# Kernel optimization log

Hardware: AMD Instinct MI355X
Metric: run time of the kernel (lower is better)

## Reference

```python
import jax, jax.numpy as jnp
import numpy as np
from jax import lax

EPS = 1e-5
K = 7
G = 4


def _dwconv_bn(x, w, g, b, m, v):
    # depthwise 3x3, pad 1, then BN (eval mode with running stats)
    C = x.shape[1]
    y = lax.conv_general_dilated(x, w, (1, 1), [(1, 1), (1, 1)],
                                 feature_group_count=C,
                                 dimension_numbers=('NCHW', 'OIHW', 'NCHW'))
    scale = (g / jnp.sqrt(v + EPS))[None, :, None, None]
    return (y - m[None, :, None, None]) * scale + b[None, :, None, None]


def _proj(t, pw1, pb1, pw2, pb2):
    # 1x1 conv -> GELU(exact) -> 1x1 conv, on small spatial maps
    h = jnp.einsum('bchw,oc->bohw', t, pw1) + pb1[None, :, None, None]
    h = jax.nn.gelu(h, approximate=False)
    return jnp.einsum('bchw,oc->bohw', h, pw2) + pb2[None, :, None, None]


def setup_inputs() -> dict:
    key = jax.random.key(0)
    ks = jax.random.split(key, 17)
    B, C, H, W = 16, 256, 56, 56
    r = C // 4
    inp = {
        'x1': jax.random.normal(ks[0], (B, C, H, W), jnp.float32),
        'dw1_w': jax.random.normal(ks[1], (C, 1, 3, 3), jnp.float32) * 0.1,
        'dw1_g': jax.random.uniform(ks[2], (C,), jnp.float32, 0.5, 1.5),
        'dw1_b': jax.random.normal(ks[3], (C,), jnp.float32) * 0.1,
        'dw1_m': jax.random.normal(ks[4], (C,), jnp.float32) * 0.1,
        'dw1_v': jax.random.uniform(ks[5], (C,), jnp.float32, 0.5, 1.5),
        'dw2_w': jax.random.normal(ks[6], (C, 1, 3, 3), jnp.float32) * 0.1,
        'dw2_g': jax.random.uniform(ks[7], (C,), jnp.float32, 0.5, 1.5),
        'dw2_b': jax.random.normal(ks[8], (C,), jnp.float32) * 0.1,
        'dw2_m': jax.random.normal(ks[9], (C,), jnp.float32) * 0.1,
        'dw2_v': jax.random.uniform(ks[10], (C,), jnp.float32, 0.5, 1.5),
        'weight1': jax.random.normal(ks[11], (G, C, K, K), jnp.float32) * 0.02,
        'bias1': jax.random.normal(ks[12], (G, C), jnp.float32) * 0.02,
        'pw1': jax.random.normal(ks[13], (r, C), jnp.float32) * 0.05,
        'pb1': jax.random.normal(ks[14], (r,), jnp.float32) * 0.05,
        'pw2': jax.random.normal(ks[15], (C * G, r), jnp.float32) * 0.05,
        'pb2': jax.random.normal(ks[16], (C * G,), jnp.float32) * 0.05,
    }
    return inp


def reference(x1, dw1_w, dw1_g, dw1_b, dw1_m, dw1_v,
              dw2_w, dw2_g, dw2_b, dw2_m, dw2_v,
              weight1, bias1, pw1, pb1, pw2, pb2):
    B, C, H, W = x1.shape
    # gated fuse: relu6(dw1(x)) * dw2(x)
    a = jnp.clip(_dwconv_bn(x1, dw1_w, dw1_g, dw1_b, dw1_m, dw1_v), 0.0, 6.0)
    x_fuse = a * _dwconv_bn(x1, dw2_w, dw2_g, dw2_b, dw2_m, dw2_v)

    # adaptive avg pool to (K,K): H,W multiples of K -> uniform block means
    pooled = x_fuse.reshape(B, C, K, H // K, K, W // K).mean(axis=(3, 5))

    # dynamic kernel: proj -> softmax over groups -> weighted sum of weight1
    scale1 = _proj(pooled, pw1, pb1, pw2, pb2).reshape(B, G, C, K, K)
    scale1 = jax.nn.softmax(scale1, axis=1)
    w_dyn = jnp.sum(scale1 * weight1[None], axis=1)  # [B, C, K, K]

    # dynamic bias
    mean_x = x_fuse.mean(axis=(-2, -1), keepdims=True)  # [B, C, 1, 1]
    sb = _proj(mean_x, pw1, pb1, pw2, pb2).reshape(B, G, C)
    sb = jax.nn.softmax(sb, axis=1)
    b_dyn = jnp.sum(sb * bias1[None], axis=1)  # [B, C]

    # per-sample depthwise conv with dynamic weights
    pad = K // 2

    def per_sample(xi, wi):  # xi [C,H,W], wi [C,K,K]
        y = lax.conv_general_dilated(xi[None], wi[:, None], (1, 1),
                                     [(pad, pad), (pad, pad)],
                                     feature_group_count=C,
                                     dimension_numbers=('NCHW', 'OIHW', 'NCHW'))
        return y[0]

    out = jax.vmap(per_sample)(x_fuse, w_dyn)  # [B, C, H, W]
    return out + b_dyn[:, :, None, None]
```

## Files before the change

kernel.cpp:

```cpp
#include <hip/hip_runtime.h>
#include <math.h>

#define BATCH 16
#define CH 256
#define HW 56
#define NPIX (HW*HW)

__device__ __forceinline__ void fuse_tile(
    const float* __restrict__ plane, int ty, int tx,
    const float w1[9], const float w2[9],
    float sc1, float be1, float sc2, float be2,
    float res[4][4])
{
    const int oy = 4 * ty;
    float y1a[4][4], y2a[4][4];
    #pragma unroll
    for (int a = 0; a < 4; a++)
        #pragma unroll
        for (int e = 0; e < 4; e++) { y1a[a][e] = 0.f; y2a[a][e] = 0.f; }

    #pragma unroll
    for (int iy = 0; iy < 6; iy++) {
        const int r    = oy - 1 + iy;
        const bool rok = (r >= 0) && (r < 56);
        const int rc   = rok ? r : 0;
        float rb[12];
        #pragma unroll
        for (int k = 0; k < 3; k++) {
            const int cx  = tx - 1 + k;
            const bool cv = (cx >= 0) && (cx < 14);
            const int cc2 = cv ? cx : 0;
            const bool ok = rok && cv;
            float4 v = *(const float4*)(plane + rc*56 + 4*cc2);
            rb[4*k+0] = ok ? v.x : 0.f;
            rb[4*k+1] = ok ? v.y : 0.f;
            rb[4*k+2] = ok ? v.z : 0.f;
            rb[4*k+3] = ok ? v.w : 0.f;
        }
        #pragma unroll
        for (int tyy = 0; tyy < 4; tyy++) {
            const int ky = iy - tyy;
            if (ky >= 0 && ky < 3) {
                #pragma unroll
                for (int e = 0; e < 4; e++)
                    #pragma unroll
                    for (int dj = 0; dj < 3; dj++) {
                        float xv = rb[3 + e + dj];
                        y1a[tyy][e] += xv * w1[ky*3+dj];
                        y2a[tyy][e] += xv * w2[ky*3+dj];
                    }
            }
        }
    }
    #pragma unroll
    for (int tyy = 0; tyy < 4; tyy++)
        #pragma unroll
        for (int e = 0; e < 4; e++) {
            float y1 = y1a[tyy][e] * sc1 + be1;
            float y2 = y2a[tyy][e] * sc2 + be2;
            float a = fminf(fmaxf(y1, 0.f), 6.f);
            res[tyy][e] = a * y2;
        }
}

#define K1_LOAD_ROW(r, dst) do {                                                 \
    const int   rr_  = (r);                                                      \
    const bool  rok_ = ((unsigned)rr_ < 56u);                                    \
    const float* rp_ = plane + (rok_ ? rr_ : 0) * 56;                            \
    float4 a_ = *(const float4*)(rp_ + col0);                                    \
    float4 b_ = *(const float4*)(rp_ + cbase + 4);                               \
    float4 c_ = *(const float4*)(rp_ + cbase + 8);                               \
    float4 d_ = *(const float4*)(rp_ + col3);                                    \
    const bool l_ = rok_ && (cx > 0);                                            \
    const bool r_ = rok_ && (cx < 6);                                            \
    (dst)[0]=l_?a_.x:0.f;  (dst)[1]=l_?a_.y:0.f;  (dst)[2]=l_?a_.z:0.f;  (dst)[3]=l_?a_.w:0.f;   \
    (dst)[4]=rok_?b_.x:0.f;(dst)[5]=rok_?b_.y:0.f;(dst)[6]=rok_?b_.z:0.f;(dst)[7]=rok_?b_.w:0.f; \
    (dst)[8]=rok_?c_.x:0.f;(dst)[9]=rok_?c_.y:0.f;(dst)[10]=rok_?c_.z:0.f;(dst)[11]=rok_?c_.w:0.f;\
    (dst)[12]=r_?d_.x:0.f; (dst)[13]=r_?d_.y:0.f; (dst)[14]=r_?d_.z:0.f; (dst)[15]=r_?d_.w:0.f; \
} while (0)

__global__ __launch_bounds__(256) void k1_cell(
    const float* __restrict__ x1,
    const float* __restrict__ dw1w, const float* __restrict__ g1, const float* __restrict__ b1,
    const float* __restrict__ m1, const float* __restrict__ v1,
    const float* __restrict__ dw2w, const float* __restrict__ g2, const float* __restrict__ b2,
    const float* __restrict__ m2, const float* __restrict__ v2,
    float* __restrict__ pooled)
{
    const int g    = blockIdx.x * 256 + threadIdx.x;
    const int bc   = g / 49;
    const int cell = g - bc * 49;
    const int c    = bc & 255;
    const int cy   = cell / 7, cx = cell - cy * 7;
    const float* plane = x1 + (size_t)bc * NPIX;

    float w1[9], w2[9];
    #pragma unroll
    for (int k = 0; k < 9; k++) { w1[k] = dw1w[c*9+k]; w2[k] = dw2w[c*9+k]; }
    const float sc1 = g1[c] * rsqrtf(v1[c] + 1e-5f);
    const float be1 = b1[c] - m1[c] * sc1;
    const float sc2 = g2[c] * rsqrtf(v2[c] + 1e-5f);
    const float be2 = b2[c] - m2[c] * sc2;

    const int rbase = 8*cy - 1;
    const int cbase = 8*cx - 4;
    const int col0  = (cx > 0) ? cbase      : 0;
    const int col3  = (cx < 6) ? cbase + 12 : 0;

    float rows[3][16];
    K1_LOAD_ROW(rbase + 0, rows[0]);
    K1_LOAD_ROW(rbase + 1, rows[1]);

    float sum = 0.f;
    #pragma unroll
    for (int yy = 0; yy < 8; yy++) {
        K1_LOAD_ROW(rbase + yy + 2, rows[(yy + 2) % 3]);
        float y1[8], y2[8];
        #pragma unroll
        for (int e = 0; e < 8; e++) { y1[e] = 0.f; y2[e] = 0.f; }
        #pragma unroll
        for (int ky = 0; ky < 3; ky++) {
            const float* rr = rows[(yy + ky) % 3];
            #pragma unroll
            for (int e = 0; e < 8; e++)
                #pragma unroll
                for (int kx = 0; kx < 3; kx++) {
                    float xv = rr[3 + e + kx];
                    y1[e] += xv * w1[ky*3+kx];
                    y2[e] += xv * w2[ky*3+kx];
                }
        }
        #pragma unroll
        for (int e = 0; e < 8; e++) {
            float a = fminf(fmaxf(y1[e]*sc1 + be1, 0.f), 6.f);
            sum += a * (y2[e]*sc2 + be2);
        }
    }
    pooled[(size_t)bc * 49 + cell] = sum * (1.f/64.f);
}

__global__ __launch_bounds__(256) void k2a(
    const float* __restrict__ pooled, const float* __restrict__ pw1,
    const float* __restrict__ pb1, float* __restrict__ h)
{
    const int b  = blockIdx.x;
    const int oc = blockIdx.y;
    const int t  = threadIdx.x;
    __shared__ float pl[256*50];

    const float* pp = pooled + (size_t)b * 256 * 49;
    for (int idx = t; idx < 256*49; idx += 256) {
        int cc = idx / 49, p = idx - cc * 49;
        pl[cc*50 + p] = pp[idx];
    }
    __syncthreads();
    {
        float s = 0.f;
        #pragma unroll
        for (int p = 0; p < 49; p++) s += pl[t*50 + p];
        pl[t*50 + 49] = s * (1.f/49.f);
    }
    __syncthreads();

    for (int idx = t; idx < 16*50; idx += 256) {
        int ol = idx / 50, p = idx - ol * 50;
        int o = oc * 16 + ol;
        const float* wrow = pw1 + o * 256;
        float acc = pb1[o];
        #pragma unroll 8
        for (int cc = 0; cc < 256; cc++) acc += wrow[cc] * pl[cc*50 + p];
        float gv = 0.5f * acc * (1.f + erff(acc * 0.70710678118654752f));
        h[((size_t)b * 50 + p) * 64 + o] = gv;
    }
}

__global__ __launch_bounds__(256) void k2b(
    const float* __restrict__ h, const float* __restrict__ pw2, const float* __restrict__ pb2,
    const float* __restrict__ weight1, const float* __restrict__ bias1,
    float* __restrict__ w_dyn, float* __restrict__ b_dyn)
{
    const int b   = blockIdx.x;
    const int cch = blockIdx.y;
    const int t   = threadIdx.x;
    const int c_base = cch * 16;

    __shared__ __attribute__((aligned(16))) float hl[50*64];
    __shared__ float sl[64*51];

    const float* hp = h + (size_t)b * 50 * 64;
    for (int i = t; i < 800; i += 256) ((float4*)hl)[i] = ((const float4*)hp)[i];

    const int row = t & 63;
    const int pb  = t >> 6;
    const int g   = row >> 4, cl = row & 15;
    const int o2  = (g << 8) + c_base + cl;

    float wreg[64];
    {
        const float4* w4 = (const float4*)(pw2 + (size_t)o2 * 64);
        #pragma unroll
        for (int r4 = 0; r4 < 16; r4++) {
            float4 v = w4[r4];
            wreg[4*r4] = v.x; wreg[4*r4+1] = v.y; wreg[4*r4+2] = v.z; wreg[4*r4+3] = v.w;
        }
    }
    const float bias2 = pb2[o2];
    __syncthreads();

    for (int p = pb; p < 50; p += 4) {
        const float4* hv = (const float4*)&hl[p*64];
        float acc = bias2;
        #pragma unroll
        for (int r4 = 0; r4 < 16; r4++) {
            float4 v = hv[r4];
            acc += wreg[4*r4]*v.x + wreg[4*r4+1]*v.y + wreg[4*r4+2]*v.z + wreg[4*r4+3]*v.w;
        }
        sl[row*51 + p] = acc;
    }
    __syncthreads();

    for (int idx = t; idx < 16*50; idx += 256) {
        int cl2 = idx / 50, p = idx - cl2 * 50;
        float s0 = sl[(cl2     )*51 + p];
        float s1 = sl[(16 + cl2)*51 + p];
        float s2 = sl[(32 + cl2)*51 + p];
        float s3 = sl[(48 + cl2)*51 + p];
        float mx = fmaxf(fmaxf(s0, s1), fmaxf(s2, s3));
        float e0 = expf(s0-mx), e1 = expf(s1-mx), e2 = expf(s2-mx), e3 = expf(s3-mx);
        float inv = 1.f / (e0+e1+e2+e3);
        e0 *= inv; e1 *= inv; e2 *= inv; e3 *= inv;
        int cc = c_base + cl2;
        if (p < 49) {
            float wv = e0*weight1[(0*256+cc)*49+p] + e1*weight1[(1*256+cc)*49+p]
                     + e2*weight1[(2*256+cc)*49+p] + e3*weight1[(3*256+cc)*49+p];
            w_dyn[((size_t)b*256 + cc)*49 + p] = wv;
        } else {
            b_dyn[b*256 + cc] = e0*bias1[cc] + e1*bias1[256+cc] + e2*bias1[512+cc] + e3*bias1[768+cc];
        }
    }
}

#define S3 68
__global__ __launch_bounds__(256) void k3_dyn(
    const float* __restrict__ x1,
    const float* __restrict__ dw1w, const float* __restrict__ g1, const float* __restrict__ b1,
    const float* __restrict__ m1, const float* __restrict__ v1,
    const float* __restrict__ dw2w, const float* __restrict__ g2, const float* __restrict__ b2,
    const float* __restrict__ m2, const float* __restrict__ v2,
    const float* __restrict__ w_dyn, const float* __restrict__ b_dyn,
    float* __restrict__ out)
{
    const int bc = blockIdx.x;
    const int c  = bc & 255;
    const int t  = threadIdx.x;
    __shared__ __attribute__((aligned(16))) float halo[62*S3];

    float w1[9], w2[9];
    #pragma unroll
    for (int k = 0; k < 9; k++) { w1[k] = dw1w[c*9+k]; w2[k] = dw2w[c*9+k]; }
    const float sc1 = g1[c] * rsqrtf(v1[c] + 1e-5f);
    const float be1 = b1[c] - m1[c] * sc1;
    const float sc2 = g2[c] * rsqrtf(v2[c] + 1e-5f);
    const float be2 = b2[c] - m2[c] * sc2;
    float wk[49];
    const float* wp = w_dyn + (size_t)bc * 49;
    #pragma unroll
    for (int k = 0; k < 49; k++) wk[k] = wp[k];
    const float bias = b_dyn[bc];
    const float* plane = x1 + (size_t)bc * NPIX;

    const int ty = t / 14, tx = t - ty * 14;

    if (t < 192) {
        float res[4][4];
        fuse_tile(plane, ty, tx, w1, w2, sc1, be1, sc2, be2, res);
        #pragma unroll
        for (int tyy = 0; tyy < 4; tyy++) {
            float4 r4; r4.x=res[tyy][0]; r4.y=res[tyy][1]; r4.z=res[tyy][2]; r4.w=res[tyy][3];
            *(float4*)&halo[(4*ty + tyy + 3)*S3 + 4 + 4*tx] = r4;
        }
    } else {
        const int lane = t - 192;
        float4 z = make_float4(0.f, 0.f, 0.f, 0.f);
        for (int task = lane; task < 208; task += 64) {
            int row, c4;
            if (task < 96) { int tr = task >> 4; row = (tr < 3) ? tr : 56 + tr; c4 = task & 15; }
            else           { int m = task - 96;  row = 3 + (m >> 1); c4 = (m & 1) ? 15 : 0; }
            *(float4*)&halo[row*S3 + 4*c4] = z;
        }
        const int tt = lane >> 4;
        const int p  = lane & 15;
        const int y  = 52 + (p >> 2);
        const int x  = 4*(10 + tt) + (p & 3);
        float y1 = 0.f, y2 = 0.f;
        #pragma unroll
        for (int ky = 0; ky < 3; ky++) {
            const int r  = y - 1 + ky;
            const bool rv = (r < 56);
            const int rc = rv ? r : 55;
            #pragma unroll
            for (int kx = 0; kx < 3; kx++) {
                const int cc2 = x - 1 + kx;
                const bool cv = (cc2 < 56);
                const float xv = (rv && cv) ? plane[rc*56 + (cv ? cc2 : 55)] : 0.f;
                y1 += xv * w1[ky*3+kx];
                y2 += xv * w2[ky*3+kx];
            }
        }
        float a = fminf(fmaxf(y1*sc1 + be1, 0.f), 6.f);
        halo[(y + 3)*S3 + 4 + x] = a * (y2*sc2 + be2);
    }
    __syncthreads();

    if (t < 192) {
        const int oy = ty * 4, ox = tx * 4;
        float acc[4][4];
        #pragma unroll
        for (int a = 0; a < 4; a++)
            #pragma unroll
            for (int bb = 0; bb < 4; bb++) acc[a][bb] = bias;

        #pragma unroll
        for (int iy = 0; iy < 10; iy++) {
            const float* hr = &halo[(oy+iy)*S3 + ox];
            float4 a = *(const float4*)hr;
            float4 b = *(const float4*)(hr + 4);
            float4 cc = *(const float4*)(hr + 8);
            float row[12];
            row[0]=a.x; row[1]=a.y; row[2]=a.z; row[3]=a.w;
            row[4]=b.x; row[5]=b.y; row[6]=b.z; row[7]=b.w;
            row[8]=cc.x; row[9]=cc.y; row[10]=cc.z; row[11]=cc.w;
            #pragma unroll
            for (int tyy = 0; tyy < 4; tyy++) {
                const int ky = iy - tyy;
                if (ky >= 0 && ky < 7) {
                    #pragma unroll
                    for (int txx = 0; txx < 4; txx++)
                        #pragma unroll
                        for (int kx = 0; kx < 7; kx++)
                            acc[tyy][txx] += row[1+txx+kx] * wk[ky*7+kx];
                }
            }
        }
        float* op = out + (size_t)bc * NPIX;
        #pragma unroll
        for (int tyy = 0; tyy < 4; tyy++) {
            float4 r4; r4.x = acc[tyy][0]; r4.y = acc[tyy][1]; r4.z = acc[tyy][2]; r4.w = acc[tyy][3];
            *(float4*)(op + (oy+tyy)*56 + ox) = r4;
        }
    } else {
        const int lane = t - 192;
        const int tt = lane >> 4;
        const int p  = lane & 15;
        const int y  = 52 + (p >> 2);
        const int x  = 4*(10 + tt) + (p & 3);
        float acc = bias;
        #pragma unroll
        for (int ky = 0; ky < 7; ky++)
            #pragma unroll
            for (int kx = 0; kx < 7; kx++)
                acc += halo[(y + ky)*S3 + (x + 1) + kx] * wk[ky*7+kx];
        out[(size_t)bc * NPIX + y*56 + x] = acc;
    }
}

extern "C" void kernel_launch(void* const* d_in, const int* in_sizes, int n_in,
                              void* d_out, int out_size, void* d_ws, size_t ws_size,
                              hipStream_t stream) {
    const float* x1    = (const float*)d_in[0];
    const float* dw1w  = (const float*)d_in[1];
    const float* dw1g  = (const float*)d_in[2];
    const float* dw1b  = (const float*)d_in[3];
    const float* dw1m  = (const float*)d_in[4];
    const float* dw1v  = (const float*)d_in[5];
    const float* dw2w  = (const float*)d_in[6];
    const float* dw2g  = (const float*)d_in[7];
    const float* dw2b  = (const float*)d_in[8];
    const float* dw2m  = (const float*)d_in[9];
    const float* dw2v  = (const float*)d_in[10];
    const float* weight1 = (const float*)d_in[11];
    const float* bias1   = (const float*)d_in[12];
    const float* pw1     = (const float*)d_in[13];
    const float* pb1     = (const float*)d_in[14];
    const float* pw2     = (const float*)d_in[15];
    const float* pb2     = (const float*)d_in[16];

    float* out = (float*)d_out;
    float* ws  = (float*)d_ws;
    float* pooled = ws;
    float* h      = ws + 200704;
    float* w_dyn  = ws + 251904;
    float* b_dyn  = ws + 452608;

    k1_cell<<<784, 256, 0, stream>>>(x1, dw1w, dw1g, dw1b, dw1m, dw1v,
                                     dw2w, dw2g, dw2b, dw2m, dw2v, pooled);
    k2a<<<dim3(BATCH, 4), 256, 0, stream>>>(pooled, pw1, pb1, h);
    k2b<<<dim3(BATCH, 16), 256, 0, stream>>>(h, pw2, pb2, weight1, bias1, w_dyn, b_dyn);
    k3_dyn<<<BATCH*CH, 256, 0, stream>>>(x1, dw1w, dw1g, dw1b, dw1m, dw1v,
                                         dw2w, dw2g, dw2b, dw2m, dw2v,
                                         w_dyn, b_dyn, out);
}
```

Baseline: 204.2 us.

## Materialize fused activation in k1 and drop recompute from dynamic conv kernel

The first kernel now writes the fused depthwise/BN/ReLU6-product map to a padded workspace buffer, with stride 68 and zeroed borders, while it computes the pooled cells. The final 7x7 dynamic conv reads that buffer directly with one thread per 4x4 tile across 3136 blocks, replacing the per-plane shared-memory halo, the 3x3 recompute and the block sync. The two small projection kernels are merged into a single kernel with one block per (batch, pooled position). This trades recompute for an extra write and read of about 63 MB of intermediate data through global memory.

```diff
diff --git a/kernel.cpp b/kernel.cpp
--- a/kernel.cpp
+++ b/kernel.cpp
@@ -6,62 +6,8 @@
 #define HW 56
 #define NPIX (HW*HW)
 
-__device__ __forceinline__ void fuse_tile(
-    const float* __restrict__ plane, int ty, int tx,
-    const float w1[9], const float w2[9],
-    float sc1, float be1, float sc2, float be2,
-    float res[4][4])
-{
-    const int oy = 4 * ty;
-    float y1a[4][4], y2a[4][4];
-    #pragma unroll
-    for (int a = 0; a < 4; a++)
-        #pragma unroll
-        for (int e = 0; e < 4; e++) { y1a[a][e] = 0.f; y2a[a][e] = 0.f; }
-
-    #pragma unroll
-    for (int iy = 0; iy < 6; iy++) {
-        const int r    = oy - 1 + iy;
-        const bool rok = (r >= 0) && (r < 56);
-        const int rc   = rok ? r : 0;
-        float rb[12];
-        #pragma unroll
-        for (int k = 0; k < 3; k++) {
-            const int cx  = tx - 1 + k;
-            const bool cv = (cx >= 0) && (cx < 14);
-            const int cc2 = cv ? cx : 0;
-            const bool ok = rok && cv;
-            float4 v = *(const float4*)(plane + rc*56 + 4*cc2);
-            rb[4*k+0] = ok ? v.x : 0.f;
-            rb[4*k+1] = ok ? v.y : 0.f;
-            rb[4*k+2] = ok ? v.z : 0.f;
-            rb[4*k+3] = ok ? v.w : 0.f;
-        }
-        #pragma unroll
-        for (int tyy = 0; tyy < 4; tyy++) {
-            const int ky = iy - tyy;
-            if (ky >= 0 && ky < 3) {
-                #pragma unroll
-                for (int e = 0; e < 4; e++)
-                    #pragma unroll
-                    for (int dj = 0; dj < 3; dj++) {
-                        float xv = rb[3 + e + dj];
-                        y1a[tyy][e] += xv * w1[ky*3+dj];
-                        y2a[tyy][e] += xv * w2[ky*3+dj];
-                    }
-            }
-        }
-    }
-    #pragma unroll
-    for (int tyy = 0; tyy < 4; tyy++)
-        #pragma unroll
-        for (int e = 0; e < 4; e++) {
-            float y1 = y1a[tyy][e] * sc1 + be1;
-            float y2 = y2a[tyy][e] * sc2 + be2;
-            float a = fminf(fmaxf(y1, 0.f), 6.f);
-            res[tyy][e] = a * y2;
-        }
-}
+#define FSTRIDE 68
+#define FPLANE (56*FSTRIDE)
 
 #define K1_LOAD_ROW(r, dst) do {                                                 \
     const int   rr_  = (r);                                                      \
@@ -85,7 +31,9 @@
     const float* __restrict__ m1, const float* __restrict__ v1,
     const float* __restrict__ dw2w, const float* __restrict__ g2, const float* __restrict__ b2,
     const float* __restrict__ m2, const float* __restrict__ v2,
-    float* __restrict__ pooled)
+    float* __restrict__ pooled,
+    float* __restrict__ xf,
+    float* __restrict__ zrow)
 {
     const int g    = blockIdx.x * 256 + threadIdx.x;
     const int bc   = g / 49;
@@ -93,6 +41,10 @@
     const int c    = bc & 255;
     const int cy   = cell / 7, cx = cell - cy * 7;
     const float* plane = x1 + (size_t)bc * NPIX;
+    float* fp = xf + (size_t)bc * FPLANE;
+
+    const float4 z4 = make_float4(0.f, 0.f, 0.f, 0.f);
+    if (g < 20) ((float4*)zrow)[g] = z4;
 
     float w1[9], w2[9];
     #pragma unroll
@@ -130,237 +82,163 @@
                     y2[e] += xv * w2[ky*3+kx];
                 }
         }
+        float f[8];
         #pragma unroll
         for (int e = 0; e < 8; e++) {
             float a = fminf(fmaxf(y1[e]*sc1 + be1, 0.f), 6.f);
-            sum += a * (y2[e]*sc2 + be2);
-        }
+            f[e] = a * (y2[e]*sc2 + be2);
+            sum += f[e];
+        }
+        float* orow = fp + (8*cy + yy) * FSTRIDE;
+        float4 q0; q0.x=f[0]; q0.y=f[1]; q0.z=f[2]; q0.w=f[3];
+        float4 q1; q1.x=f[4]; q1.y=f[5]; q1.z=f[6]; q1.w=f[7];
+        *(float4*)(orow + 4 + 8*cx)     = q0;
+        *(float4*)(orow + 4 + 8*cx + 4) = q1;
+        if (cx == 0) *(float4*)(orow + 0)  = z4;
+        if (cx == 6) { *(float4*)(orow + 60) = z4; *(float4*)(orow + 64) = z4; }
     }
     pooled[(size_t)bc * 49 + cell] = sum * (1.f/64.f);
 }
 
-__global__ __launch_bounds__(256) void k2a(
-    const float* __restrict__ pooled, const float* __restrict__ pw1,
-    const float* __restrict__ pb1, float* __restrict__ h)
+__global__ __launch_bounds__(256) void k2_fused(
+    const float* __restrict__ pooled,
+    const float* __restrict__ pw1, const float* __restrict__ pb1,
+    const float* __restrict__ pw2, const float* __restrict__ pb2,
+    const float* __restrict__ weight1, const float* __restrict__ bias1,
+    float* __restrict__ w_dyn,
+    float* __restrict__ b_dyn)
 {
-    const int b  = blockIdx.x;
-    const int oc = blockIdx.y;
-    const int t  = threadIdx.x;
-    __shared__ float pl[256*50];
-
-    const float* pp = pooled + (size_t)b * 256 * 49;
-    for (int idx = t; idx < 256*49; idx += 256) {
-        int cc = idx / 49, p = idx - cc * 49;
-        pl[cc*50 + p] = pp[idx];
+    const int blk = blockIdx.x;
+    const int b = blk / 50, p = blk - b * 50;
+    const int t = threadIdx.x;
+
+    __shared__ __attribute__((aligned(16))) float xs[268];
+    __shared__ __attribute__((aligned(16))) float hs[64];
+
+    {
+        const float* pp = pooled + ((size_t)b * 256 + t) * 49;
+        float v;
+        if (p < 49) {
+            v = pp[p];
+        } else {
+            float s = 0.f;
+            #pragma unroll
+            for (int q = 0; q < 49; q++) s += pp[q];
+            v = s * (1.f/49.f);
+        }
+        xs[t + 4*(t>>6)] = v;
     }
     __syncthreads();
-    {
-        float s = 0.f;
-        #pragma unroll
-        for (int p = 0; p < 49; p++) s += pl[t*50 + p];
-        pl[t*50 + 49] = s * (1.f/49.f);
+
+    {
+        const int o = t >> 2, part = t & 3;
+        const float4* w4 = (const float4*)(pw1 + o*256 + part*64);
+        const float4* x4 = (const float4*)(xs + part*68);
+        float acc = 0.f;
+        #pragma unroll
+        for (int i = 0; i < 16; i++) {
+            float4 w = w4[i];
+            float4 x = x4[i];
+            acc += w.x*x.x + w.y*x.y + w.z*x.z + w.w*x.w;
+        }
+        acc += __shfl_xor(acc, 1);
+        acc += __shfl_xor(acc, 2);
+        if (part == 0) {
+            float zv = acc + pb1[o];
+            hs[o] = 0.5f * zv * (1.f + erff(zv * 0.70710678118654752f));
+        }
     }
     __syncthreads();
 
-    for (int idx = t; idx < 16*50; idx += 256) {
-        int ol = idx / 50, p = idx - ol * 50;
-        int o = oc * 16 + ol;
-        const float* wrow = pw1 + o * 256;
-        float acc = pb1[o];
-        #pragma unroll 8
-        for (int cc = 0; cc < 256; cc++) acc += wrow[cc] * pl[cc*50 + p];
-        float gv = 0.5f * acc * (1.f + erff(acc * 0.70710678118654752f));
-        h[((size_t)b * 50 + p) * 64 + o] = gv;
-    }
-}
-
-__global__ __launch_bounds__(256) void k2b(
-    const float* __restrict__ h, const float* __restrict__ pw2, const float* __restrict__ pb2,
-    const float* __restrict__ weight1, const float* __restrict__ bias1,
-    float* __restrict__ w_dyn, float* __restrict__ b_dyn)
-{
-    const int b   = blockIdx.x;
-    const int cch = blockIdx.y;
-    const int t   = threadIdx.x;
-    const int c_base = cch * 16;
-
-    __shared__ __attribute__((aligned(16))) float hl[50*64];
-    __shared__ float sl[64*51];
-
-    const float* hp = h + (size_t)b * 50 * 64;
-    for (int i = t; i < 800; i += 256) ((float4*)hl)[i] = ((const float4*)hp)[i];
-
-    const int row = t & 63;
-    const int pb  = t >> 6;
-    const int g   = row >> 4, cl = row & 15;
-    const int o2  = (g << 8) + c_base + cl;
-
-    float wreg[64];
-    {
-        const float4* w4 = (const float4*)(pw2 + (size_t)o2 * 64);
-        #pragma unroll
-        for (int r4 = 0; r4 < 16; r4++) {
-            float4 v = w4[r4];
-            wreg[4*r4] = v.x; wreg[4*r4+1] = v.y; wreg[4*r4+2] = v.z; wreg[4*r4+3] = v.w;
-        }
-    }
-    const float bias2 = pb2[o2];
-    __syncthreads();
-
-    for (int p = pb; p < 50; p += 4) {
-        const float4* hv = (const float4*)&hl[p*64];
-        float acc = bias2;
-        #pragma unroll
-        for (int r4 = 0; r4 < 16; r4++) {
-            float4 v = hv[r4];
-            acc += wreg[4*r4]*v.x + wreg[4*r4+1]*v.y + wreg[4*r4+2]*v.z + wreg[4*r4+3]*v.w;
-        }
-        sl[row*51 + p] = acc;
-    }
-    __syncthreads();
-
-    for (int idx = t; idx < 16*50; idx += 256) {
-        int cl2 = idx / 50, p = idx - cl2 * 50;
-        float s0 = sl[(cl2     )*51 + p];
-        float s1 = sl[(16 + cl2)*51 + p];
-        float s2 = sl[(32 + cl2)*51 + p];
-        float s3 = sl[(48 + cl2)*51 + p];
-        float mx = fmaxf(fmaxf(s0, s1), fmaxf(s2, s3));
-        float e0 = expf(s0-mx), e1 = expf(s1-mx), e2 = expf(s2-mx), e3 = expf(s3-mx);
+    {
+        float s[4];
+        #pragma unroll
+        for (int gg = 0; gg < 4; gg++) {
+            const int o2 = (gg << 8) + t;
+            const float4* w4 = (const float4*)(pw2 + (size_t)o2 * 64);
+            float acc = pb2[o2];
+            #pragma unroll
+            for (int j = 0; j < 16; j++) {
+                float4 w = w4[j];
+                const float4 h = *(const float4*)(hs + 4*j);
+                acc += w.x*h.x + w.y*h.y + w.z*h.z + w.w*h.w;
+            }
+            s[gg] = acc;
+        }
+        float mx = fmaxf(fmaxf(s[0], s[1]), fmaxf(s[2], s[3]));
+        float e0 = expf(s[0]-mx), e1 = expf(s[1]-mx), e2 = expf(s[2]-mx), e3 = expf(s[3]-mx);
         float inv = 1.f / (e0+e1+e2+e3);
         e0 *= inv; e1 *= inv; e2 *= inv; e3 *= inv;
-        int cc = c_base + cl2;
         if (p < 49) {
-            float wv = e0*weight1[(0*256+cc)*49+p] + e1*weight1[(1*256+cc)*49+p]
-                     + e2*weight1[(2*256+cc)*49+p] + e3*weight1[(3*256+cc)*49+p];
-            w_dyn[((size_t)b*256 + cc)*49 + p] = wv;
+            float wv = e0*weight1[(0*256+t)*49+p] + e1*weight1[(1*256+t)*49+p]
+                     + e2*weight1[(2*256+t)*49+p] + e3*weight1[(3*256+t)*49+p];
+            w_dyn[((size_t)b*256 + t)*64 + p] = wv;
         } else {
-            b_dyn[b*256 + cc] = e0*bias1[cc] + e1*bias1[256+cc] + e2*bias1[512+cc] + e3*bias1[768+cc];
-        }
-    }
-}
-
-#define S3 68
-__global__ __launch_bounds__(256) void k3_dyn(
-    const float* __restrict__ x1,
-    const float* __restrict__ dw1w, const float* __restrict__ g1, const float* __restrict__ b1,
-    const float* __restrict__ m1, const float* __restrict__ v1,
-    const float* __restrict__ dw2w, const float* __restrict__ g2, const float* __restrict__ b2,
-    const float* __restrict__ m2, const float* __restrict__ v2,
+            b_dyn[b*256 + t] = e0*bias1[t] + e1*bias1[256+t] + e2*bias1[512+t] + e3*bias1[768+t];
+        }
+    }
+}
+
+__global__ __launch_bounds__(256) void k3_direct(
+    const float* __restrict__ xf, const float* __restrict__ zrow,
     const float* __restrict__ w_dyn, const float* __restrict__ b_dyn,
     float* __restrict__ out)
 {
-    const int bc = blockIdx.x;
-    const int c  = bc & 255;
-    const int t  = threadIdx.x;
-    __shared__ __attribute__((aligned(16))) float halo[62*S3];
-
-    float w1[9], w2[9];
-    #pragma unroll
-    for (int k = 0; k < 9; k++) { w1[k] = dw1w[c*9+k]; w2[k] = dw2w[c*9+k]; }
-    const float sc1 = g1[c] * rsqrtf(v1[c] + 1e-5f);
-    const float be1 = b1[c] - m1[c] * sc1;
-    const float sc2 = g2[c] * rsqrtf(v2[c] + 1e-5f);
-    const float be2 = b2[c] - m2[c] * sc2;
-    float wk[49];
-    const float* wp = w_dyn + (size_t)bc * 49;
-    #pragma unroll
-    for (int k = 0; k < 49; k++) wk[k] = wp[k];
+    const int g  = blockIdx.x * 256 + threadIdx.x;
+    const int bc = g / 196;
+    const int tl = g - bc * 196;
+    const int ty = tl / 14, tx = tl - ty * 14;
+    const int oy = ty * 4, ox = tx * 4;
+    const float* fp = xf + (size_t)bc * FPLANE;
+
+    float wk[52];
+    {
+        const float4* w4 = (const float4*)(w_dyn + (size_t)bc * 64);
+        #pragma unroll
+        for (int i = 0; i < 13; i++) {
+            float4 v = w4[i];
+            wk[4*i]=v.x; wk[4*i+1]=v.y; wk[4*i+2]=v.z; wk[4*i+3]=v.w;
+        }
+    }
     const float bias = b_dyn[bc];
-    const float* plane = x1 + (size_t)bc * NPIX;
-
-    const int ty = t / 14, tx = t - ty * 14;
-
-    if (t < 192) {
-        float res[4][4];
-        fuse_tile(plane, ty, tx, w1, w2, sc1, be1, sc2, be2, res);
+
+    float acc[4][4];
+    #pragma unroll
+    for (int a = 0; a < 4; a++)
+        #pragma unroll
+        for (int bb = 0; bb < 4; bb++) acc[a][bb] = bias;
+
+    #pragma unroll
+    for (int iy = 0; iy < 10; iy++) {
+        const int r = oy - 3 + iy;
+        const float* rp = ((unsigned)r < 56u) ? (fp + r * FSTRIDE) : zrow;
+        float4 A = *(const float4*)(rp + ox);
+        float4 B = *(const float4*)(rp + ox + 4);
+        float4 C = *(const float4*)(rp + ox + 8);
+        float4 D = *(const float4*)(rp + ox + 12);
+        float row[16];
+        row[0]=A.x; row[1]=A.y; row[2]=A.z; row[3]=A.w;
+        row[4]=B.x; row[5]=B.y; row[6]=B.z; row[7]=B.w;
+        row[8]=C.x; row[9]=C.y; row[10]=C.z; row[11]=C.w;
+        row[12]=D.x; row[13]=D.y; row[14]=D.z; row[15]=D.w;
         #pragma unroll
         for (int tyy = 0; tyy < 4; tyy++) {
-            float4 r4; r4.x=res[tyy][0]; r4.y=res[tyy][1]; r4.z=res[tyy][2]; r4.w=res[tyy][3];
-            *(float4*)&halo[(4*ty + tyy + 3)*S3 + 4 + 4*tx] = r4;
-        }
-    } else {
-        const int lane = t - 192;
-        float4 z = make_float4(0.f, 0.f, 0.f, 0.f);
-        for (int task = lane; task < 208; task += 64) {
-            int row, c4;
-            if (task < 96) { int tr = task >> 4; row = (tr < 3) ? tr : 56 + tr; c4 = task & 15; }
-            else           { int m = task - 96;  row = 3 + (m >> 1); c4 = (m & 1) ? 15 : 0; }
-            *(float4*)&halo[row*S3 + 4*c4] = z;
-        }
-        const int tt = lane >> 4;
-        const int p  = lane & 15;
-        const int y  = 52 + (p >> 2);
-        const int x  = 4*(10 + tt) + (p & 3);
-        float y1 = 0.f, y2 = 0.f;
-        #pragma unroll
-        for (int ky = 0; ky < 3; ky++) {
-            const int r  = y - 1 + ky;
-            const bool rv = (r < 56);
-            const int rc = rv ? r : 55;
-            #pragma unroll
-            for (int kx = 0; kx < 3; kx++) {
-                const int cc2 = x - 1 + kx;
-                const bool cv = (cc2 < 56);
-                const float xv = (rv && cv) ? plane[rc*56 + (cv ? cc2 : 55)] : 0.f;
-                y1 += xv * w1[ky*3+kx];
-                y2 += xv * w2[ky*3+kx];
+            const int ky = iy - tyy;
+            if (ky >= 0 && ky < 7) {
+                #pragma unroll
+                for (int txx = 0; txx < 4; txx++)
+                    #pragma unroll
+                    for (int kx = 0; kx < 7; kx++)
+                        acc[tyy][txx] += row[1 + txx + kx] * wk[ky*7 + kx];
             }
         }
-        float a = fminf(fmaxf(y1*sc1 + be1, 0.f), 6.f);
-        halo[(y + 3)*S3 + 4 + x] = a * (y2*sc2 + be2);
-    }
-    __syncthreads();
-
-    if (t < 192) {
-        const int oy = ty * 4, ox = tx * 4;
-        float acc[4][4];
-        #pragma unroll
-        for (int a = 0; a < 4; a++)
-            #pragma unroll
-            for (int bb = 0; bb < 4; bb++) acc[a][bb] = bias;
-
-        #pragma unroll
-        for (int iy = 0; iy < 10; iy++) {
-            const float* hr = &halo[(oy+iy)*S3 + ox];
-            float4 a = *(const float4*)hr;
-            float4 b = *(const float4*)(hr + 4);
-            float4 cc = *(const float4*)(hr + 8);
-            float row[12];
-            row[0]=a.x; row[1]=a.y; row[2]=a.z; row[3]=a.w;
-            row[4]=b.x; row[5]=b.y; row[6]=b.z; row[7]=b.w;
-            row[8]=cc.x; row[9]=cc.y; row[10]=cc.z; row[11]=cc.w;
-            #pragma unroll
-            for (int tyy = 0; tyy < 4; tyy++) {
-                const int ky = iy - tyy;
-                if (ky >= 0 && ky < 7) {
-                    #pragma unroll
-                    for (int txx = 0; txx < 4; txx++)
-                        #pragma unroll
-                        for (int kx = 0; kx < 7; kx++)
-                            acc[tyy][txx] += row[1+txx+kx] * wk[ky*7+kx];
-                }
-            }
-        }
-        float* op = out + (size_t)bc * NPIX;
-        #pragma unroll
-        for (int tyy = 0; tyy < 4; tyy++) {
-            float4 r4; r4.x = acc[tyy][0]; r4.y = acc[tyy][1]; r4.z = acc[tyy][2]; r4.w = acc[tyy][3];
-            *(float4*)(op + (oy+tyy)*56 + ox) = r4;
-        }
-    } else {
-        const int lane = t - 192;
-        const int tt = lane >> 4;
-        const int p  = lane & 15;
-        const int y  = 52 + (p >> 2);
-        const int x  = 4*(10 + tt) + (p & 3);
-        float acc = bias;
-        #pragma unroll
-        for (int ky = 0; ky < 7; ky++)
-            #pragma unroll
-            for (int kx = 0; kx < 7; kx++)
-                acc += halo[(y + ky)*S3 + (x + 1) + kx] * wk[ky*7+kx];
-        out[(size_t)bc * NPIX + y*56 + x] = acc;
+    }
+
+    float* op = out + (size_t)bc * NPIX;
+    #pragma unroll
+    for (int tyy = 0; tyy < 4; tyy++) {
+        float4 r4; r4.x = acc[tyy][0]; r4.y = acc[tyy][1]; r4.z = acc[tyy][2]; r4.w = acc[tyy][3];
+        *(float4*)(op + (oy+tyy)*56 + ox) = r4;
     }
 }
 
@@ -388,15 +266,15 @@
     float* out = (float*)d_out;
     float* ws  = (float*)d_ws;
     float* pooled = ws;
-    float* h      = ws + 200704;
-    float* w_dyn  = ws + 251904;
-    float* b_dyn  = ws + 452608;
+    float* w_dyn  = ws + 200704;
+    float* b_dyn  = ws + 462848;
+    float* zrow   = ws + 466944;
+    float* xf     = ws + 467024;
 
     k1_cell<<<784, 256, 0, stream>>>(x1, dw1w, dw1g, dw1b, dw1m, dw1v,
-                                     dw2w, dw2g, dw2b, dw2m, dw2v, pooled);
-    k2a<<<dim3(BATCH, 4), 256, 0, stream>>>(pooled, pw1, pb1, h);
-    k2b<<<dim3(BATCH, 16), 256, 0, stream>>>(h, pw2, pb2, weight1, bias1, w_dyn, b_dyn);
-    k3_dyn<<<BATCH*CH, 256, 0, stream>>>(x1, dw1w, dw1g, dw1b, dw1m, dw1v,
-                                         dw2w, dw2g, dw2b, dw2m, dw2v,
-                                         w_dyn, b_dyn, out);
-}
+                                     dw2w, dw2g, dw2b, dw2m, dw2v,
+                                     pooled, xf, zrow);
+    k2_fused<<<800, 256, 0, stream>>>(pooled, pw1, pb1, pw2, pb2,
+                                      weight1, bias1, w_dyn, b_dyn);
+    k3_direct<<<3136, 256, 0, stream>>>(xf, zrow, w_dyn, b_dyn, out);
+}
```

New measurement: 245.7 us. 1.2x slower.
